# Kernel tuning notes

Hardware: AMD Instinct MI355X
Metric: run time of the kernel (lower is better)

## Reference

```python
import jax, jax.numpy as jnp
import numpy as np

B, C, H, W_SP = 64, 16, 8, 8
IN_DIM, MIDDLE, NUM_CLASSES = 2048, 8192, 2048
K_ITERS, TAU, NUM_GROUPS = 1024, 0.5, 8
SPLIT = NUM_GROUPS * 7 * 7  # 392
BN_EPS = 1e-5


def setup_inputs() -> dict:
    key = jax.random.key(0)
    ks = jax.random.split(key, 20)
    f = jax.random.normal(ks[0], (B, C, H, W_SP), jnp.float32)

    def lin(kw, kb, fan_out, fan_in):
        lim = 1.0 / np.sqrt(fan_in)
        W = jax.random.uniform(kw, (fan_out, fan_in), jnp.float32, -lim, lim)
        b = jax.random.uniform(kb, (fan_out,), jnp.float32, -lim, lim)
        return W, b

    def bn_stats(km, kv, n):
        rm = 0.1 * jax.random.normal(km, (n,), jnp.float32)
        rv = jax.random.uniform(kv, (n,), jnp.float32, 0.5, 1.5)
        return rm, rv

    W1, b1 = lin(ks[1], ks[2], MIDDLE, IN_DIM)
    g1 = 1.0 + 0.1 * jax.random.normal(ks[3], (MIDDLE,), jnp.float32)
    beta1 = 0.1 * jax.random.normal(ks[4], (MIDDLE,), jnp.float32)
    rm1, rv1 = bn_stats(ks[5], ks[6], MIDDLE)

    W2, b2 = lin(ks[7], ks[8], MIDDLE, MIDDLE)
    g2 = 1.0 + 0.1 * jax.random.normal(ks[9], (MIDDLE,), jnp.float32)
    beta2 = 0.1 * jax.random.normal(ks[10], (MIDDLE,), jnp.float32)
    rm2, rv2 = bn_stats(ks[11], ks[12], MIDDLE)

    W3, b3 = lin(ks[13], ks[14], NUM_CLASSES, MIDDLE)
    rm3, rv3 = bn_stats(ks[15], ks[16], NUM_CLASSES)  # final BN, affine=False

    return {"f": f, "W1": W1, "b1": b1, "g1": g1, "beta1": beta1, "rm1": rm1, "rv1": rv1,
            "W2": W2, "b2": b2, "g2": g2, "beta2": beta2, "rm2": rm2, "rv2": rv2,
            "W3": W3, "b3": b3, "rm3": rm3, "rv3": rv3}


def _bn(x, rm, rv, g=None, b=None):
    y = (x - rm) / jnp.sqrt(rv + BN_EPS)
    if g is not None:
        y = y * g + b
    return y


def reference(f, W1, b1, g1, beta1, rm1, rv1, W2, b2, g2, beta2, rm2, rv2, W3, b3, rm3, rv3):
    # FFT over spatial axes; the original code overwrites abs/angle with the raw
    # complex array twice, then the torch dtype cast drops the imaginary part.
    f_fft = jnp.fft.fft2(f, axes=(2, 3))
    flat = jnp.real(f_fft).reshape(B, -1).astype(f.dtype)  # [64, 1024]
    x = jnp.concatenate([flat, flat], axis=1)              # [64, 2048]

    # MLP in eval mode (Dropout = identity, BatchNorm uses running stats)
    h = jax.nn.relu(_bn(x @ W1.T + b1, rm1, rv1, g1, beta1))
    h = jax.nn.relu(_bn(h @ W2.T + b2, rm2, rv2, g2, beta2))
    mask = _bn(h @ W3.T + b3, rm3, rv3)                    # [64, 2048]

    # Iterated gumbel-softmax with running max, k=1024 iterations
    keys = jax.random.split(jax.random.key(42), K_ITERS)
    tiny = jnp.finfo(mask.dtype).tiny

    def step(carry, k):
        m, z = carry
        u = jax.random.uniform(k, m.shape, m.dtype, minval=tiny, maxval=1.0)
        gum = -jnp.log(-jnp.log(u))
        m = jax.nn.softmax((m + gum) / TAU, axis=1)
        z = jnp.maximum(m, z)
        return (m, z), None

    (_, z), _ = jax.lax.scan(step, (mask, jnp.zeros_like(mask)), keys)
    return z[:, :SPLIT], z[:, SPLIT:]
```

## Files before the change

kernel.cpp:

```cpp
#include <hip/hip_runtime.h>
#include <hip/hip_bf16.h>
#include <stdint.h>

__device__ __forceinline__ uint32_t rotl32(uint32_t v, int s) {
    return (v << s) | (v >> (32 - s));
}

__device__ __forceinline__ void tf2x32(uint32_t k0, uint32_t k1,
                                       uint32_t x0, uint32_t x1,
                                       uint32_t& o0, uint32_t& o1) {
    uint32_t ks2 = k0 ^ k1 ^ 0x1BD11BDAu;
    x0 += k0; x1 += k1;
#define TFR(R0,R1,R2,R3) \
    x0 += x1; x1 = rotl32(x1, R0); x1 ^= x0; \
    x0 += x1; x1 = rotl32(x1, R1); x1 ^= x0; \
    x0 += x1; x1 = rotl32(x1, R2); x1 ^= x0; \
    x0 += x1; x1 = rotl32(x1, R3); x1 ^= x0;
    TFR(13,15,26,6)   x0 += k1;  x1 += ks2 + 1u;
    TFR(17,29,16,24)  x0 += ks2; x1 += k0  + 2u;
    TFR(13,15,26,6)   x0 += k0;  x1 += k1  + 3u;
    TFR(17,29,16,24)  x0 += k1;  x1 += ks2 + 4u;
    TFR(13,15,26,6)   x0 += ks2; x1 += k0  + 5u;
#undef TFR
    o0 = x0; o1 = x1;
}

__device__ __forceinline__ uint32_t pbits32(uint32_t k0, uint32_t k1, uint32_t ctr) {
    uint32_t o0, o1;
    tf2x32(k0, k1, 0u, ctr, o0, o1);
    return o0 ^ o1;
}

#define NROW 64
#define NCOL 2048
#define NFLAT 131072
#define SPLIT 392
#define C2 2.8853900817779268f

__device__ __forceinline__ float gumbel_from_bits(uint32_t bits) {
    const float TINY = 1.17549435e-38f;
    float f = (float)(bits >> 9) * 1.1920928955078125e-7f;
    float u = fmaxf(TINY, f + TINY);
    return -logf(-logf(u));
}

template<int CTRL, int RM>
__device__ __forceinline__ float dpp_add(float s) {
    int x = __builtin_amdgcn_update_dpp(0, __builtin_bit_cast(int, s),
                                        CTRL, RM, 0xf, true);
    return s + __builtin_bit_cast(float, x);
}

__device__ __forceinline__ float wave_sum64(float v) {
    v = dpp_add<0x111, 0xf>(v);
    v = dpp_add<0x112, 0xf>(v);
    v = dpp_add<0x114, 0xf>(v);
    v = dpp_add<0x118, 0xf>(v);
    v = dpp_add<0x142, 0xa>(v);
    v = dpp_add<0x143, 0xc>(v);
    return __builtin_bit_cast(float,
        __builtin_amdgcn_readlane(__builtin_bit_cast(int, v), 63));
}

__global__ __launch_bounds__(256) void keygenF(uint32_t* __restrict__ kb) {
    int n = blockIdx.x * 256 + threadIdx.x;
    uint32_t o0, o1;
    tf2x32(0u, 42u, 0u, (uint32_t)n, o0, o1);
    kb[2 * n] = o0;
    kb[2 * n + 1] = o1;
}

__device__ __constant__ float c_ctab[8] = {
    1.0f, 0.70710678118654752f, 0.0f, -0.70710678118654752f,
   -1.0f, -0.70710678118654752f, 0.0f, 0.70710678118654752f
};

__global__ __launch_bounds__(256) void fft_x(const float* __restrict__ f,
                                             float* __restrict__ x) {
    int gid = blockIdx.x * 256 + threadIdx.x;
    int b = gid >> 10, i = gid & 1023;
    int c = i >> 6, h = (i >> 3) & 7, w = i & 7;
    const float* fb = f + ((b << 4) + c) * 64;
    float s = 0.0f;
#pragma unroll
    for (int hp = 0; hp < 8; ++hp) {
#pragma unroll
        for (int wp = 0; wp < 8; ++wp)
            s += fb[hp * 8 + wp] * c_ctab[(h * hp + w * wp) & 7];
    }
    x[b * NCOL + i] = s;
    x[b * NCOL + 1024 + i] = s;
}

__global__ __launch_bounds__(256) void prep(
    const float* __restrict__ b1, const float* __restrict__ g1,
    const float* __restrict__ be1, const float* __restrict__ rm1, const float* __restrict__ rv1,
    const float* __restrict__ b2, const float* __restrict__ g2,
    const float* __restrict__ be2, const float* __restrict__ rm2, const float* __restrict__ rv2,
    float* __restrict__ s1, float* __restrict__ o1,
    float* __restrict__ s2, float* __restrict__ o2) {
    int i = blockIdx.x * 256 + threadIdx.x;
    const float eps = 1e-5f;
    float inv = 1.0f / sqrtf(rv1[i] + eps);
    float s = g1[i] * inv;
    s1[i] = s; o1[i] = (b1[i] - rm1[i]) * s + be1[i];
    inv = 1.0f / sqrtf(rv2[i] + eps);
    s = g2[i] * inv;
    s2[i] = s; o2[i] = (b2[i] - rm2[i]) * s + be2[i];
}

template<bool AFF>
__global__ __launch_bounds__(256)
void gemm_ks(const float* __restrict__ A,
             const float* __restrict__ sA, const float* __restrict__ oA,
             const float* __restrict__ B, float* __restrict__ Cpart,
             int K, int Kc, int N) {
    __shared__ __align__(16) float As[64 * 36];
    __shared__ __align__(16) float Bs[128 * 36];
    const int t = threadIdx.x;
    const int n0 = blockIdx.x * 128;
    const int k0 = blockIdx.y * Kc;
    const int tm = t >> 4, tn = t & 15;

    float acc[4][8];
#pragma unroll
    for (int i = 0; i < 4; ++i)
#pragma unroll
        for (int j = 0; j < 8; ++j) acc[i][j] = 0.0f;

    for (int kt = k0; kt < k0 + Kc; kt += 32) {
#pragma unroll
        for (int h = 0; h < 2; ++h) {
            int idx = h * 1024 + t * 4;
            int am = idx >> 5, ak = idx & 31;
            float4 v = *(const float4*)(A + (size_t)am * K + kt + ak);
            if (AFF) {
                float4 s = *(const float4*)(sA + kt + ak);
                float4 o = *(const float4*)(oA + kt + ak);
                v.x = fmaxf(v.x * s.x + o.x, 0.0f);
                v.y = fmaxf(v.y * s.y + o.y, 0.0f);
                v.z = fmaxf(v.z * s.z + o.z, 0.0f);
                v.w = fmaxf(v.w * s.w + o.w, 0.0f);
            }
            *(float4*)&As[am * 36 + (ak ^ (((am >> 2) & 7) << 2))] = v;
        }
#pragma unroll
        for (int h = 0; h < 4; ++h) {
            int idx = h * 1024 + t * 4;
            int bn = idx >> 5, bk = idx & 31;
            float4 v = *(const float4*)(B + (size_t)(n0 + bn) * K + kt + bk);
            *(float4*)&Bs[bn * 36 + (bk ^ (((bn >> 3) & 7) << 2))] = v;
        }
        __syncthreads();
#pragma unroll
        for (int kbk = 0; kbk < 8; ++kbk) {
            float4 a[4], b[8];
            int acol = (kbk * 4) ^ ((tm & 7) << 2);
#pragma unroll
            for (int i = 0; i < 4; ++i)
                a[i] = *(const float4*)&As[(tm * 4 + i) * 36 + acol];
            int bcol = (kbk * 4) ^ ((tn & 7) << 2);
#pragma unroll
            for (int j = 0; j < 8; ++j)
                b[j] = *(const float4*)&Bs[(tn * 8 + j) * 36 + bcol];
#pragma unroll
            for (int i = 0; i < 4; ++i)
#pragma unroll
                for (int j = 0; j < 8; ++j) {
                    acc[i][j] = fmaf(a[i].x, b[j].x, acc[i][j]);
                    acc[i][j] = fmaf(a[i].y, b[j].y, acc[i][j]);
                    acc[i][j] = fmaf(a[i].z, b[j].z, acc[i][j]);
                    acc[i][j] = fmaf(a[i].w, b[j].w, acc[i][j]);
                }
        }
        __syncthreads();
    }
#pragma unroll
    for (int i = 0; i < 4; ++i) {
        size_t co = (size_t)blockIdx.y * ((size_t)64 * N)
                  + (size_t)((tm << 2) + i) * N + n0 + (tn << 3);
        float4 v0 = {acc[i][0], acc[i][1], acc[i][2], acc[i][3]};
        float4 v1 = {acc[i][4], acc[i][5], acc[i][6], acc[i][7]};
        *(float4*)(Cpart + co) = v0;
        *(float4*)(Cpart + co + 4) = v1;
    }
}

__global__ __launch_bounds__(256) void combineP(const float* __restrict__ parts,
                                                float* __restrict__ dst,
                                                int P, int total) {
    int gid = blockIdx.x * 256 + threadIdx.x;
    if (gid >= total) return;
    float s = 0.0f;
    for (int p = 0; p < P; ++p) s += parts[(size_t)p * total + gid];
    dst[gid] = s;
}

__global__ __launch_bounds__(256) void combine3(const float* __restrict__ parts,
                                                const float* __restrict__ b3,
                                                const float* __restrict__ rm3,
                                                const float* __restrict__ rv3,
                                                float* __restrict__ mstate, int P) {
    int gid = blockIdx.x * 256 + threadIdx.x;
    int c = gid & 2047;
    float v = 0.0f;
    for (int p = 0; p < P; ++p) v += parts[(size_t)p * NFLAT + gid];
    mstate[gid] = (v + b3[c] - rm3[c]) / sqrtf(rv3[c] + 1e-5f);
}

__global__ __launch_bounds__(1024)
void hash_chunk(const uint32_t* __restrict__ kb, float* __restrict__ gbuf,
                int t0, int Tc) {
    size_t total = (size_t)Tc * NFLAT;
    for (size_t idx = (size_t)blockIdx.x * 1024 + threadIdx.x; idx < total;
         idx += (size_t)gridDim.x * 1024) {
        int tt = (int)(idx >> 17);
        int j  = (int)(idx & (NFLAT - 1));
        int tg = t0 + tt;
        uint32_t k0 = kb[2 * tg], k1 = kb[2 * tg + 1];
        gbuf[idx] = gumbel_from_bits(pbits32(k0, k1, (uint32_t)j)) * C2;
    }
}

__global__ __launch_bounds__(1024)
void scan_fused(float* __restrict__ mstate, float* __restrict__ zstate,
                const float* __restrict__ gscan,
                float* __restrict__ hdst, int ht0, int hcnt,
                const uint32_t* __restrict__ kb,
                int t0, int Tc, int last, float* __restrict__ out) {
    const int tid = threadIdx.x;

    if (blockIdx.x >= 64) {
        if (hcnt <= 0) return;
        int hb = blockIdx.x - 64;
        size_t total = (size_t)hcnt * NFLAT;
        for (size_t idx = (size_t)hb * 1024 + tid; idx < total;
             idx += (size_t)192 * 1024) {
            int tt = (int)(idx >> 17);
            int j  = (int)(idx & (NFLAT - 1));
            int tg = ht0 + tt;
            uint32_t k0 = kb[2 * tg], k1 = kb[2 * tg + 1];
            hdst[idx] = gumbel_from_bits(pbits32(k0, k1, (uint32_t)j)) * C2;
        }
        return;
    }

    __shared__ __align__(16) float red[2][16];
    const int r = blockIdx.x;
    const int c0 = tid, c1 = tid + 1024;
    const int base = r * NCOL;
    float m0 = mstate[base + c0], m1 = mstate[base + c1];
    float z0, z1;
    if (t0 == 0) { z0 = 0.0f; z1 = 0.0f; }
    else         { z0 = zstate[base + c0]; z1 = zstate[base + c1]; }
    const int lane = tid & 63, wid = tid >> 6;

    float g0 = gscan[base + c0];
    float g1 = gscan[base + c1];
    for (int tt = 0; tt < Tc; ++tt) {
        float cg0 = g0, cg1 = g1;
        if (tt + 1 < Tc) {
            size_t ao = (size_t)(tt + 1) * NFLAT + base;
            g0 = gscan[ao + c0];
            g1 = gscan[ao + c1];
        }
        float p0 = exp2f(fmaf(m0, C2, cg0));
        float p1 = exp2f(fmaf(m1, C2, cg1));
        float ws = wave_sum64(p0 + p1);
        if (lane == 0) red[tt & 1][wid] = ws;
        __syncthreads();
        float S;
        {
            const float4* r4 = (const float4*)&red[tt & 1][0];
            float4 v0 = r4[0], v1 = r4[1], v2 = r4[2], v3 = r4[3];
            S = ((v0.x + v0.y) + (v0.z + v0.w)) + ((v1.x + v1.y) + (v1.z + v1.w))
              + ((v2.x + v2.y) + (v2.z + v2.w)) + ((v3.x + v3.y) + (v3.z + v3.w));
        }
        float rs = __builtin_amdgcn_rcpf(S);
        m0 = p0 * rs; m1 = p1 * rs;
        z0 = fmaxf(z0, m0); z1 = fmaxf(z1, m1);
    }
    mstate[base + c0] = m0; mstate[base + c1] = m1;
    zstate[base + c0] = z0; zstate[base + c1] = z1;
    if (last) {
        if (c0 < SPLIT) out[r * SPLIT + c0] = z0;
        else out[64 * SPLIT + r * (NCOL - SPLIT) + (c0 - SPLIT)] = z0;
        out[64 * SPLIT + r * (NCOL - SPLIT) + (c1 - SPLIT)] = z1;
    }
}

__global__ __launch_bounds__(1024)
void scan_inline(const float* __restrict__ mstate, const uint32_t* __restrict__ kb,
                 float* __restrict__ out) {
    const int r = blockIdx.x;
    const int tid = threadIdx.x;
    const int c0 = tid, c1 = tid + 1024;
    const int base = r * NCOL;
    float m0 = mstate[base + c0], m1 = mstate[base + c1];
    float z0 = 0.0f, z1 = 0.0f;
    __shared__ __align__(16) float red[2][16];
    const int lane = tid & 63, wid = tid >> 6;

    for (int t = 0; t < 1024; ++t) {
        uint32_t k0 = kb[2 * t], k1 = kb[2 * t + 1];
        float g0 = gumbel_from_bits(pbits32(k0, k1, (uint32_t)(base + c0)));
        float g1 = gumbel_from_bits(pbits32(k0, k1, (uint32_t)(base + c1)));
        float p0 = exp2f((m0 + g0) * C2);
        float p1 = exp2f((m1 + g1) * C2);
        float ws = wave_sum64(p0 + p1);
        if (lane == 0) red[t & 1][wid] = ws;
        __syncthreads();
        float S;
        {
            const float4* r4 = (const float4*)&red[t & 1][0];
            float4 v0 = r4[0], v1 = r4[1], v2 = r4[2], v3 = r4[3];
            S = ((v0.x + v0.y) + (v0.z + v0.w)) + ((v1.x + v1.y) + (v1.z + v1.w))
              + ((v2.x + v2.y) + (v2.z + v2.w)) + ((v3.x + v3.y) + (v3.z + v3.w));
        }
        float rs = __builtin_amdgcn_rcpf(S);
        m0 = p0 * rs; m1 = p1 * rs;
        z0 = fmaxf(z0, m0); z1 = fmaxf(z1, m1);
    }
    if (c0 < SPLIT) out[r * SPLIT + c0] = z0;
    else out[64 * SPLIT + r * (NCOL - SPLIT) + (c0 - SPLIT)] = z0;
    out[64 * SPLIT + r * (NCOL - SPLIT) + (c1 - SPLIT)] = z1;
}

extern "C" void kernel_launch(void* const* d_in, const int* in_sizes, int n_in,
                              void* d_out, int out_size, void* d_ws, size_t ws_size,
                              hipStream_t stream) {
    const float* f   = (const float*)d_in[0];
    const float* W1  = (const float*)d_in[1];
    const float* b1  = (const float*)d_in[2];
    const float* g1  = (const float*)d_in[3];
    const float* be1 = (const float*)d_in[4];
    const float* rm1 = (const float*)d_in[5];
    const float* rv1 = (const float*)d_in[6];
    const float* W2  = (const float*)d_in[7];
    const float* b2  = (const float*)d_in[8];
    const float* g2  = (const float*)d_in[9];
    const float* be2 = (const float*)d_in[10];
    const float* rm2 = (const float*)d_in[11];
    const float* rv2 = (const float*)d_in[12];
    const float* W3  = (const float*)d_in[13];
    const float* b3  = (const float*)d_in[14];
    const float* rm3 = (const float*)d_in[15];
    const float* rv3 = (const float*)d_in[16];
    float* out = (float*)d_out;

    float* ws = (float*)d_ws;
    size_t off = 0;
    auto alloc = [&](size_t n) { float* p = ws + off; off += n; return p; };

    uint32_t* keybuf = (uint32_t*)alloc(2048);
    float* s1 = alloc(8192); float* o1 = alloc(8192);
    float* s2 = alloc(8192); float* o2 = alloc(8192);
    float* x      = alloc(64 * 2048);
    float* h1     = alloc((size_t)64 * 8192);
    float* h2     = alloc((size_t)64 * 8192);
    float* mstate = alloc(NFLAT);
    float* zstate = alloc(NFLAT);
    size_t fixed = off;
    float* pbuf = ws + fixed;
    size_t region = (ws_size / 4 > fixed) ? (ws_size / 4 - fixed) : 0;

    const size_t HN = (size_t)64 * 8192;
    const size_t GALL = (size_t)1024 * NFLAT;

    keygenF<<<dim3(4), 256, 0, stream>>>(keybuf);
    prep<<<dim3(32), 256, 0, stream>>>(b1, g1, be1, rm1, rv1,
                                       b2, g2, be2, rm2, rv2,
                                       s1, o1, s2, o2);
    fft_x<<<dim3(256), 256, 0, stream>>>(f, x);

    if (region >= GALL + 32 * HN) {
        float* gbufAll = pbuf;
        float* parts   = pbuf + GALL;

        gemm_ks<false><<<dim3(64, 16), 256, 0, stream>>>(
            x, nullptr, nullptr, W1, parts, 2048, 128, 8192);
        combineP<<<dim3(2048), 256, 0, stream>>>(parts, h1, 16, (int)HN);
        gemm_ks<true><<<dim3(64, 32), 256, 0, stream>>>(
            h1, s1, o1, W2, parts, 8192, 256, 8192);
        combineP<<<dim3(2048), 256, 0, stream>>>(parts, h2, 32, (int)HN);
        gemm_ks<true><<<dim3(16, 32), 256, 0, stream>>>(
            h2, s2, o2, W3, parts, 8192, 256, 2048);
        combine3<<<dim3(512), 256, 0, stream>>>(parts, b3, rm3, rv3, mstate, 32);

        hash_chunk<<<dim3(256), 1024, 0, stream>>>(keybuf, gbufAll, 0, 256);
        for (int ch = 0; ch < 8; ++ch) {
            int hstart = 256 + ch * 128;
            int hcnt = (hstart < 1024) ? 128 : 0;
            scan_fused<<<dim3(256), 1024, 0, stream>>>(
                mstate, zstate, gbufAll + (size_t)ch * 128 * NFLAT,
                gbufAll + (size_t)hstart * NFLAT, hstart, hcnt, keybuf,
                ch * 128, 128, (ch == 7) ? 1 : 0, out);
        }
    } else {
        int KS1 = (region >= 8 * HN) ? 8 : (region >= 4 * HN) ? 4 :
                  (region >= 2 * HN) ? 2 : 1;
        int KS2 = (region >= 16 * HN) ? 16 : (region >= 8 * HN) ? 8 :
                  (region >= 4 * HN) ? 4 : (region >= 2 * HN) ? 2 : 1;
        int KS3 = (region >= 16 * (size_t)NFLAT) ? 16 :
                  (region >= 8 * (size_t)NFLAT) ? 8 :
                  (region >= 4 * (size_t)NFLAT) ? 4 :
                  (region >= 2 * (size_t)NFLAT) ? 2 : 1;
        int Tc = 0;
        const int cands[5] = {128, 64, 32, 16, 8};
        for (int ci = 0; ci < 5; ++ci)
            if (2 * (size_t)cands[ci] * NFLAT <= region) { Tc = cands[ci]; break; }

        gemm_ks<false><<<dim3(64, KS1), 256, 0, stream>>>(
            x, nullptr, nullptr, W1, (KS1 > 1) ? pbuf : h1, 2048, 2048 / KS1, 8192);
        if (KS1 > 1) combineP<<<dim3(2048), 256, 0, stream>>>(pbuf, h1, KS1, (int)HN);

        gemm_ks<true><<<dim3(64, KS2), 256, 0, stream>>>(
            h1, s1, o1, W2, (KS2 > 1) ? pbuf : h2, 8192, 8192 / KS2, 8192);
        if (KS2 > 1) combineP<<<dim3(2048), 256, 0, stream>>>(pbuf, h2, KS2, (int)HN);

        if (KS3 > 1) {
            gemm_ks<true><<<dim3(16, KS3), 256, 0, stream>>>(
                h2, s2, o2, W3, pbuf, 8192, 8192 / KS3, 2048);
            combine3<<<dim3(512), 256, 0, stream>>>(pbuf, b3, rm3, rv3, mstate, KS3);
        } else {
            gemm_ks<true><<<dim3(16, 1), 256, 0, stream>>>(
                h2, s2, o2, W3, h1, 8192, 8192, 2048);
            combine3<<<dim3(512), 256, 0, stream>>>(h1, b3, rm3, rv3, mstate, 1);
        }

        if (Tc > 0) {
            float* gbuf0 = pbuf;
            float* gbuf1 = pbuf + (size_t)Tc * NFLAT;
            int NC = 1024 / Tc;
            hash_chunk<<<dim3(256), 1024, 0, stream>>>(keybuf, gbuf0, 0, Tc);
            for (int ch = 0; ch < NC; ++ch) {
                float* ga = (ch & 1) ? gbuf1 : gbuf0;
                float* gb = (ch & 1) ? gbuf0 : gbuf1;
                int last = (ch == NC - 1) ? 1 : 0;
                scan_fused<<<dim3(256), 1024, 0, stream>>>(
                    mstate, zstate, ga, gb, (ch + 1) * Tc, last ? 0 : Tc,
                    keybuf, ch * Tc, Tc, last, out);
            }
        } else {
            scan_inline<<<dim3(64), 1024, 0, stream>>>(mstate, keybuf, out);
        }
    }
}
```

Baseline: 962.3 us.

## Shrink scan blocks to 256 threads with 8 columns per thread

```diff
diff --git a/kernel.cpp b/kernel.cpp
--- a/kernel.cpp
+++ b/kernel.cpp
@@ -222,7 +222,7 @@
     }
 }
 
-__global__ __launch_bounds__(1024)
+__global__ __launch_bounds__(256)
 void scan_fused(float* __restrict__ mstate, float* __restrict__ zstate,
                 const float* __restrict__ gscan,
                 float* __restrict__ hdst, int ht0, int hcnt,
@@ -233,9 +233,10 @@
     if (blockIdx.x >= 64) {
         if (hcnt <= 0) return;
         int hb = blockIdx.x - 64;
+        int hBlocks = gridDim.x - 64;
         size_t total = (size_t)hcnt * NFLAT;
-        for (size_t idx = (size_t)hb * 1024 + tid; idx < total;
-             idx += (size_t)192 * 1024) {
+        for (size_t idx = (size_t)hb * 256 + tid; idx < total;
+             idx += (size_t)hBlocks * 256) {
             int tt = (int)(idx >> 17);
             int j  = (int)(idx & (NFLAT - 1));
             int tg = ht0 + tt;
@@ -245,47 +246,73 @@
         return;
     }
 
-    __shared__ __align__(16) float red[2][16];
     const int r = blockIdx.x;
-    const int c0 = tid, c1 = tid + 1024;
     const int base = r * NCOL;
-    float m0 = mstate[base + c0], m1 = mstate[base + c1];
-    float z0, z1;
-    if (t0 == 0) { z0 = 0.0f; z1 = 0.0f; }
-    else         { z0 = zstate[base + c0]; z1 = zstate[base + c1]; }
+    const int c = tid * 8;
     const int lane = tid & 63, wid = tid >> 6;
-
-    float g0 = gscan[base + c0];
-    float g1 = gscan[base + c1];
+    __shared__ __align__(16) float red[2][4];
+
+    float m[8], z[8];
+    {
+        float4 a = *(const float4*)&mstate[base + c];
+        float4 b = *(const float4*)&mstate[base + c + 4];
+        m[0]=a.x; m[1]=a.y; m[2]=a.z; m[3]=a.w;
+        m[4]=b.x; m[5]=b.y; m[6]=b.z; m[7]=b.w;
+    }
+    if (t0 == 0) {
+#pragma unroll
+        for (int k = 0; k < 8; ++k) z[k] = 0.0f;
+    } else {
+        float4 a = *(const float4*)&zstate[base + c];
+        float4 b = *(const float4*)&zstate[base + c + 4];
+        z[0]=a.x; z[1]=a.y; z[2]=a.z; z[3]=a.w;
+        z[4]=b.x; z[5]=b.y; z[6]=b.z; z[7]=b.w;
+    }
+
+    float4 ga = *(const float4*)&gscan[base + c];
+    float4 gb = *(const float4*)&gscan[base + c + 4];
+
     for (int tt = 0; tt < Tc; ++tt) {
-        float cg0 = g0, cg1 = g1;
+        float g[8] = {ga.x, ga.y, ga.z, ga.w, gb.x, gb.y, gb.z, gb.w};
         if (tt + 1 < Tc) {
-            size_t ao = (size_t)(tt + 1) * NFLAT + base;
-            g0 = gscan[ao + c0];
-            g1 = gscan[ao + c1];
-        }
-        float p0 = exp2f(fmaf(m0, C2, cg0));
-        float p1 = exp2f(fmaf(m1, C2, cg1));
-        float ws = wave_sum64(p0 + p1);
+            size_t ao = (size_t)(tt + 1) * NFLAT + base + c;
+            ga = *(const float4*)&gscan[ao];
+            gb = *(const float4*)&gscan[ao + 4];
+        }
+        float p[8];
+#pragma unroll
+        for (int k = 0; k < 8; ++k) p[k] = exp2f(fmaf(m[k], C2, g[k]));
+        float s = ((p[0] + p[1]) + (p[2] + p[3])) + ((p[4] + p[5]) + (p[6] + p[7]));
+        float ws = wave_sum64(s);
         if (lane == 0) red[tt & 1][wid] = ws;
         __syncthreads();
-        float S;
-        {
-            const float4* r4 = (const float4*)&red[tt & 1][0];
-            float4 v0 = r4[0], v1 = r4[1], v2 = r4[2], v3 = r4[3];
-            S = ((v0.x + v0.y) + (v0.z + v0.w)) + ((v1.x + v1.y) + (v1.z + v1.w))
-              + ((v2.x + v2.y) + (v2.z + v2.w)) + ((v3.x + v3.y) + (v3.z + v3.w));
-        }
+        float S = (red[tt & 1][0] + red[tt & 1][1])
+                + (red[tt & 1][2] + red[tt & 1][3]);
         float rs = __builtin_amdgcn_rcpf(S);
-        m0 = p0 * rs; m1 = p1 * rs;
-        z0 = fmaxf(z0, m0); z1 = fmaxf(z1, m1);
-    }
-    mstate[base + c0] = m0; mstate[base + c1] = m1;
-    zstate[base + c0] = z0; zstate[base + c1] = z1;
+#pragma unroll
+        for (int k = 0; k < 8; ++k) {
+            m[k] = p[k] * rs;
+            z[k] = fmaxf(z[k], m[k]);
+        }
+    }
+
+    {
+        float4 a = {m[0], m[1], m[2], m[3]};
+        float4 b = {m[4], m[5], m[6], m[7]};
+        *(float4*)&mstate[base + c] = a;
+        *(float4*)&mstate[base + c + 4] = b;
+        a = {z[0], z[1], z[2], z[3]};
+        b = {z[4], z[5], z[6], z[7]};
+        *(float4*)&zstate[base + c] = a;
+        *(float4*)&zstate[base + c + 4] = b;
+    }
     if (last) {
-        if (c0 < SPLIT) out[r * SPLIT + c0] = z0;
-        else out[64 * SPLIT + r * (NCOL - SPLIT) + (c0 - SPLIT)] = z0;
-        out[64 * SPLIT + r * (NCOL - SPLIT) + (c1 - SPLIT)] = z1;
+#pragma unroll
+        for (int k = 0; k < 8; ++k) {
+            int cc = c + k;
+            if (cc < SPLIT) out[r * SPLIT + cc] = z[k];
+            else out[64 * SPLIT + r * (NCOL - SPLIT) + (cc - SPLIT)] = z[k];
+        }
     }
 }
 
@@ -380,18 +407,18 @@
         gemm_ks<false><<<dim3(64, 16), 256, 0, stream>>>(
             x, nullptr, nullptr, W1, parts, 2048, 128, 8192);
         combineP<<<dim3(2048), 256, 0, stream>>>(parts, h1, 16, (int)HN);
-        gemm_ks<true><<<dim3(64, 32), 256, 0, stream>>>(
-            h1, s1, o1, W2, parts, 8192, 256, 8192);
-        combineP<<<dim3(2048), 256, 0, stream>>>(parts, h2, 32, (int)HN);
+        gemm_ks<true><<<dim3(64, 16), 256, 0, stream>>>(
+            h1, s1, o1, W2, parts, 8192, 512, 8192);
+        combineP<<<dim3(2048), 256, 0, stream>>>(parts, h2, 16, (int)HN);
         gemm_ks<true><<<dim3(16, 32), 256, 0, stream>>>(
             h2, s2, o2, W3, parts, 8192, 256, 2048);
         combine3<<<dim3(512), 256, 0, stream>>>(parts, b3, rm3, rv3, mstate, 32);
 
-        hash_chunk<<<dim3(256), 1024, 0, stream>>>(keybuf, gbufAll, 0, 256);
+        hash_chunk<<<dim3(256), 1024, 0, stream>>>(keybuf, gbufAll, 0, 128);
         for (int ch = 0; ch < 8; ++ch) {
-            int hstart = 256 + ch * 128;
+            int hstart = (ch + 1) * 128;
             int hcnt = (hstart < 1024) ? 128 : 0;
-            scan_fused<<<dim3(256), 1024, 0, stream>>>(
+            scan_fused<<<dim3(320), 256, 0, stream>>>(
                 mstate, zstate, gbufAll + (size_t)ch * 128 * NFLAT,
                 gbufAll + (size_t)hstart * NFLAT, hstart, hcnt, keybuf,
                 ch * 128, 128, (ch == 7) ? 1 : 0, out);
@@ -437,7 +464,7 @@
                 float* ga = (ch & 1) ? gbuf1 : gbuf0;
                 float* gb = (ch & 1) ? gbuf0 : gbuf1;
                 int last = (ch == NC - 1) ? 1 : 0;
-                scan_fused<<<dim3(256), 1024, 0, stream>>>(
+                scan_fused<<<dim3(320), 256, 0, stream>>>(
                     mstate, zstate, ga, gb, (ch + 1) * Tc, last ? 0 : Tc,
                     keybuf, ch * Tc, Tc, last, out);
             }
```

Measured after the change: 1.225 ms. 1.27x slower.
